# Kernel optimization log

Measured on AMD Instinct MI355X. Metric: run time of the kernel, lower is better.

## Reference

```python
import jax, jax.numpy as jnp
import numpy as np

NUM_ROUTES, NUM_TIME, DIM, K, C = 100000, 2016, 256, 100, 5
BATCH = 262144


def _xavier(key, shape):
    fan_in, fan_out = shape[0], shape[1]
    lim = np.sqrt(6.0 / (fan_in + fan_out))
    return jax.random.uniform(key, shape, jnp.float32, -lim, lim)


def setup_inputs() -> dict:
    key = jax.random.key(0)
    ks = jax.random.split(key, 9)
    route_idx = jax.random.randint(ks[0], (BATCH,), 0, NUM_ROUTES)
    time_idx = jax.random.randint(ks[1], (BATCH,), 0, NUM_TIME)
    route_table = _xavier(ks[2], (NUM_ROUTES, DIM))
    time_table = _xavier(ks[3], (NUM_TIME, DIM))
    w = _xavier(ks[4], (DIM, K))
    mode_a = _xavier(ks[5], (DIM, C))
    mode_b = _xavier(ks[6], (DIM, C))
    mode_bias = jnp.zeros((C, C), jnp.float32)
    fc_lim = 1.0 / np.sqrt(C * C + K)
    fc_w = jax.random.uniform(ks[7], (C * C + K, 1), jnp.float32, -fc_lim, fc_lim)
    fc_b = jax.random.uniform(ks[8], (1,), jnp.float32, -fc_lim, fc_lim)
    return {
        "route_idx": route_idx, "time_idx": time_idx,
        "route_table": route_table, "time_table": time_table,
        "w": w, "mode_a": mode_a, "mode_b": mode_b,
        "mode_bias": mode_bias, "fc_w": fc_w, "fc_b": fc_b,
    }


def reference(route_idx, time_idx, route_table, time_table, w, mode_a, mode_b, mode_bias, fc_w, fc_b):
    r = route_table[route_idx]            # [B, D]
    t = time_table[time_idx]              # [B, D]
    gcp = jax.nn.relu((r * t) @ w)        # [B, K]
    # einsum('ni,nj->nij') then contracting i with mode_a and j with mode_b
    # equals outer product of the two small projections (exact same math):
    ra = r @ mode_a                       # [B, C]
    tb = t @ mode_b                       # [B, C]
    inter = jax.nn.sigmoid(ra[:, :, None] * tb[:, None, :] + mode_bias)  # [B, C, C]
    feats = jnp.concatenate([gcp, inter.reshape(inter.shape[0], -1)], axis=1)  # [B, K + C*C]
    out = feats @ fc_w + fc_b             # [B, 1]
    return jnp.squeeze(out, axis=-1)      # [B]
```

## Files before the change

### kernel.cpp

```cpp
#include <hip/hip_runtime.h>
#include <stdint.h>

#define BATCH   262144
#define NROUTES 100000
#define NTIME   2016
#define DIM     256
#define KOUT    100
#define NTILES  7

typedef __attribute__((ext_vector_type(2))) float f32x2;
typedef __attribute__((ext_vector_type(4))) float f32x4;

#define WS_WFRAG_BYTES ((size_t)(NTILES * 8 * 64 * 8))
#define WS_RA_OFF   (WS_WFRAG_BYTES)
#define WS_TB_OFF   (WS_RA_OFF + (size_t)NROUTES * 32)
#define WS_RT8_OFF  (WS_TB_OFF + (size_t)NTIME * 32)
#define WS_TT8_OFF  (WS_RT8_OFF + (size_t)NROUTES * 256)
#define WS_NEED     (WS_TT8_OFF + (size_t)NTIME * 256)

template<int CTRL>
static __device__ __forceinline__ float dpp_add(float x) {
  int s = __builtin_amdgcn_update_dpp(0, __builtin_bit_cast(int, x), CTRL, 0xF, 0xF, true);
  return x + __builtin_bit_cast(float, s);
}
static __device__ __forceinline__ float wave_sum63(float x) {
  x = dpp_add<0x111>(x);
  x = dpp_add<0x112>(x);
  x = dpp_add<0x114>(x);
  x = dpp_add<0x118>(x);
  x = dpp_add<0x142>(x);
  x = dpp_add<0x143>(x);
  return x;
}
static __device__ __forceinline__ float sum16_all(float x) {
  x = dpp_add<0x0B1>(x);
  x = dpp_add<0x04E>(x);
  x = dpp_add<0x124>(x);
  x = dpp_add<0x128>(x);
  return x;
}
static __device__ __forceinline__ float sigm(float z) {
  return __builtin_amdgcn_rcpf(1.0f + __expf(-z));
}

template<int DO8>
__global__ __launch_bounds__(256) void prep_kernel(
    const float* __restrict__ route_table,
    const float* __restrict__ time_table,
    const float* __restrict__ w,
    const float* __restrict__ mode_a,
    const float* __restrict__ mode_b,
    uint8_t* __restrict__ ws)
{
  const int b   = blockIdx.x;
  const int tid = threadIdx.x;

  if (b < 14) {
    const int u = b * 256 + tid;
    const int lane = u & 63;
    const int frag = u >> 6;
    const int ks = frag / NTILES;
    const int nt = frag % NTILES;
    const int n  = nt * 16 + (lane & 15);
    const int k0 = ks * 32 + (lane >> 4) * 8;
    float v[8];
    #pragma unroll
    for (int j = 0; j < 8; ++j)
      v[j] = (n < KOUT) ? w[(size_t)(k0 + j) * KOUT + n] : 0.0f;
    uint32_t d0 = 0, d1 = 0;
    d0 = __builtin_amdgcn_cvt_pk_fp8_f32(v[0], v[1], d0, false);
    d0 = __builtin_amdgcn_cvt_pk_fp8_f32(v[2], v[3], d0, true);
    d1 = __builtin_amdgcn_cvt_pk_fp8_f32(v[4], v[5], d1, false);
    d1 = __builtin_amdgcn_cvt_pk_fp8_f32(v[6], v[7], d1, true);
    ((uint2*)ws)[u] = make_uint2(d0, d1);
    return;
  }

  const float* tab; const float* proj; float* outp; uint8_t* out8; int base;
  if (b < 14 + 63) {
    tab = time_table;  proj = mode_b; outp = (float*)(ws + WS_TB_OFF);
    out8 = ws + WS_TT8_OFF; base = (b - 14) * 32;
  } else {
    tab = route_table; proj = mode_a; outp = (float*)(ws + WS_RA_OFF);
    out8 = ws + WS_RT8_OFF; base = (b - 77) * 32;
  }

  const int wave = tid >> 6, lane = tid & 63;
  const int perm = (2 * (lane >> 4) + ((lane >> 1) & 1)) * 8 +
                   ((lane >> 2) & 3) * 2 + (lane & 1);

  float A[4][5];
  #pragma unroll
  for (int j = 0; j < 4; ++j)
    #pragma unroll
    for (int i = 0; i < 5; ++i)
      A[j][i] = proj[(4 * perm + j) * 5 + i];

  const int row0 = base + wave * 8;
  float4 v[8];
  #pragma unroll
  for (int rr = 0; rr < 8; ++rr)
    v[rr] = *(const float4*)(tab + (size_t)(row0 + rr) * DIM + 4 * perm);

  #pragma unroll
  for (int rr = 0; rr < 8; ++rr) {
    const int row = row0 + rr;
    if (DO8) {
      uint32_t u = 0;
      u = __builtin_amdgcn_cvt_pk_fp8_f32(8.f * v[rr].x, 8.f * v[rr].y, u, false);
      u = __builtin_amdgcn_cvt_pk_fp8_f32(8.f * v[rr].z, 8.f * v[rr].w, u, true);
      *(uint32_t*)(out8 + (size_t)row * 256 + 4 * lane) = u;
    }
    float p[5];
    #pragma unroll
    for (int i = 0; i < 5; ++i) {
      float s = v[rr].x * A[0][i] + v[rr].y * A[1][i] + v[rr].z * A[2][i] + v[rr].w * A[3][i];
      p[i] = wave_sum63(s);
    }
    if (lane == 63) {
      float* o = outp + (size_t)row * 8;
      *(f32x4*)o = (f32x4){p[0], p[1], p[2], p[3]};
      o[4] = p[4];
    }
  }
}

__global__ __launch_bounds__(256, 3) void main_pipelined(
    const int*   __restrict__ route_idx,
    const int*   __restrict__ time_idx,
    const float* __restrict__ mode_bias,
    const float* __restrict__ fc_w,
    const float* __restrict__ fc_b,
    const uint8_t* __restrict__ ws,
    float* __restrict__ out)
{
  __shared__ uint4 wlds[1792];
  const int tid  = threadIdx.x;
  const int wave = tid >> 6, lane = tid & 63;
  const int col  = lane & 15, quad = lane >> 4;
  const int base = (blockIdx.x * 4 + wave) * 64;

  int ri[4], ti[4];
  #pragma unroll
  for (int t = 0; t < 4; ++t) {
    ri[t] = route_idx[base + t * 16 + col];
    ti[t] = time_idx[base + t * 16 + col];
  }

  {
    const uint4* wsrc = (const uint4*)ws;
    #pragma unroll
    for (int j = 0; j < 7; ++j)
      wlds[j * 256 + tid] = wsrc[j * 256 + tid];
  }

  float fcw_l[NTILES];
  #pragma unroll
  for (int nt = 0; nt < NTILES; ++nt) {
    const int n = nt * 16 + col;
    fcw_l[nt] = (n < KOUT) ? fc_w[n] * 0.015625f : 0.0f;
  }
  const float fb = fc_b[0];

  uint4 rw[2][4], tw[2][4];
  auto issue = [&](int buf, int t) {
    const uint8_t* rb = ws + WS_RT8_OFF + (size_t)ri[t] * 256 + quad * 16;
    const uint8_t* tb = ws + WS_TT8_OFF + (size_t)ti[t] * 256 + quad * 16;
    #pragma unroll
    for (int i = 0; i < 4; ++i) {
      rw[buf][i] = *(const uint4*)(rb + i * 64);
      tw[buf][i] = *(const uint4*)(tb + i * 64);
    }
  };

  issue(0, 0);
  __syncthreads();

  const uint2* wl2 = (const uint2*)wlds;

  #pragma unroll
  for (int it = 0; it < 4; ++it) {
    const int cb = it & 1, nb = cb ^ 1;

    const float* rap = (const float*)(ws + WS_RA_OFF) + (size_t)ri[it] * 8;
    const float* tbp = (const float*)(ws + WS_TB_OFF) + (size_t)ti[it] * 8;
    f32x4 ra0 = *(const f32x4*)rap; float ra4 = rap[4];
    f32x4 tb0 = *(const f32x4*)tbp; float tb4 = tbp[4];
    if (it < 3) issue(nb, it + 1);

    f32x4 acc[NTILES];
    #pragma unroll
    for (int nt = 0; nt < NTILES; ++nt) acc[nt] = (f32x4){0.f, 0.f, 0.f, 0.f};

    #pragma unroll
    for (int ks = 0; ks < 8; ++ks) {
      const int i = ks >> 1;
      const uint32_t ra = (ks & 1) ? rw[cb][i].z : rw[cb][i].x;
      const uint32_t rb = (ks & 1) ? rw[cb][i].w : rw[cb][i].y;
      const uint32_t ta = (ks & 1) ? tw[cb][i].z : tw[cb][i].x;
      const uint32_t tb = (ks & 1) ? tw[cb][i].w : tw[cb][i].y;
      f32x2 r01 = __builtin_amdgcn_cvt_pk_f32_fp8(ra, false);
      f32x2 r23 = __builtin_amdgcn_cvt_pk_f32_fp8(ra, true);
      f32x2 r45 = __builtin_amdgcn_cvt_pk_f32_fp8(rb, false);
      f32x2 r67 = __builtin_amdgcn_cvt_pk_f32_fp8(rb, true);
      f32x2 t01 = __builtin_amdgcn_cvt_pk_f32_fp8(ta, false);
      f32x2 t23 = __builtin_amdgcn_cvt_pk_f32_fp8(ta, true);
      f32x2 t45 = __builtin_amdgcn_cvt_pk_f32_fp8(tb, false);
      f32x2 t67 = __builtin_amdgcn_cvt_pk_f32_fp8(tb, true);
      f32x2 x01 = r01 * t01, x23 = r23 * t23, x45 = r45 * t45, x67 = r67 * t67;
      uint32_t p0 = 0, p1 = 0;
      p0 = __builtin_amdgcn_cvt_pk_fp8_f32(x01.x, x01.y, p0, false);
      p0 = __builtin_amdgcn_cvt_pk_fp8_f32(x23.x, x23.y, p0, true);
      p1 = __builtin_amdgcn_cvt_pk_fp8_f32(x45.x, x45.y, p1, false);
      p1 = __builtin_amdgcn_cvt_pk_fp8_f32(x67.x, x67.y, p1, true);
      const long a64 = __builtin_bit_cast(long, make_uint2(p0, p1));
      #pragma unroll
      for (int nt = 0; nt < NTILES; ++nt) {
        const long b64 = __builtin_bit_cast(long, wl2[(ks * NTILES + nt) * 64 + lane]);
        acc[nt] = __builtin_amdgcn_mfma_f32_16x16x32_fp8_fp8(a64, b64, acc[nt], 0, 0, 0);
      }
    }

    float s[4];
    #pragma unroll
    for (int reg = 0; reg < 4; ++reg) {
      float v = 0.f;
      #pragma unroll
      for (int nt = 0; nt < NTILES; ++nt)
        v += fmaxf(acc[nt][reg], 0.f) * fcw_l[nt];
      s[reg] = sum16_all(v);
    }

    const float rav[5] = {ra0.x, ra0.y, ra0.z, ra0.w, ra4};
    const float tbv[5] = {tb0.x, tb0.y, tb0.z, tb0.w, tb4};
    const float rq = (quad & 2) ? ((quad & 1) ? rav[3] : rav[2])
                                : ((quad & 1) ? rav[1] : rav[0]);
    const float tq = (quad & 2) ? ((quad & 1) ? tbv[3] : tbv[2])
                                : ((quad & 1) ? tbv[1] : tbv[0]);
    float sig = 0.f;
    #pragma unroll
    for (int j = 0; j < 5; ++j)
      sig += sigm(rq * tbv[j] + mode_bias[5 * quad + j]) * fc_w[KOUT + 5 * quad + j];
    sig += sigm(rav[4] * tq + mode_bias[20 + quad]) * fc_w[KOUT + 20 + quad];
    if (quad == 0)
      sig += sigm(rav[4] * tbv[4] + mode_bias[24]) * fc_w[KOUT + 24];
    sig += __shfl_xor(sig, 16, 64);
    sig += __shfl_xor(sig, 32, 64);

    if (quad == (col >> 2)) {
      const float sa = (col & 1) ? s[1] : s[0];
      const float sb = (col & 1) ? s[3] : s[2];
      const float gcp = (col & 2) ? sb : sa;
      out[base + it * 16 + col] = fb + gcp + sig;
    }
  }
}

__global__ __launch_bounds__(256, 4) void main_fallback(
    const int*   __restrict__ route_idx,
    const int*   __restrict__ time_idx,
    const float* __restrict__ route_table,
    const float* __restrict__ time_table,
    const float* __restrict__ mode_bias,
    const float* __restrict__ fc_w,
    const float* __restrict__ fc_b,
    const uint8_t* __restrict__ ws,
    float* __restrict__ out)
{
  __shared__ uint4 wlds[1792];
  const int tid  = threadIdx.x;
  const int wave = tid >> 6, lane = tid & 63;
  const int col  = lane & 15, quad = lane >> 4;
  const int m0   = blockIdx.x * 64 + wave * 16;
  const size_t ri = (size_t)route_idx[m0 + col];
  const size_t ti = (size_t)time_idx[m0 + col];

  const float* rap = (const float*)(ws + WS_RA_OFF) + ri * 8;
  const float* tbp = (const float*)(ws + WS_TB_OFF) + ti * 8;
  f32x4 ra0 = *(const f32x4*)rap; float ra4 = rap[4];
  f32x4 tb0 = *(const f32x4*)tbp; float tb4 = tbp[4];

  {
    const uint4* wsrc = (const uint4*)ws;
    #pragma unroll
    for (int j = 0; j < 7; ++j)
      wlds[j * 256 + tid] = wsrc[j * 256 + tid];
  }
  __syncthreads();

  float fcw_l[NTILES];
  #pragma unroll
  for (int nt = 0; nt < NTILES; ++nt) {
    const int n = nt * 16 + col;
    fcw_l[nt] = (n < KOUT) ? fc_w[n] * 0.015625f : 0.0f;
  }

  f32x4 acc[NTILES];
  #pragma unroll
  for (int nt = 0; nt < NTILES; ++nt) acc[nt] = (f32x4){0.f, 0.f, 0.f, 0.f};
  const uint2* wl2 = (const uint2*)wlds;

  #pragma unroll
  for (int ks = 0; ks < 8; ++ks) {
    const float4* rp = (const float4*)(route_table + ri * DIM + ks * 32 + quad * 8);
    const float4* tp = (const float4*)(time_table  + ti * DIM + ks * 32 + quad * 8);
    float4 r0 = rp[0], r1 = rp[1], t0 = tp[0], t1 = tp[1];
    uint32_t p0 = 0, p1 = 0;
    p0 = __builtin_amdgcn_cvt_pk_fp8_f32(64.f * r0.x * t0.x, 64.f * r0.y * t0.y, p0, false);
    p0 = __builtin_amdgcn_cvt_pk_fp8_f32(64.f * r0.z * t0.z, 64.f * r0.w * t0.w, p0, true);
    p1 = __builtin_amdgcn_cvt_pk_fp8_f32(64.f * r1.x * t1.x, 64.f * r1.y * t1.y, p1, false);
    p1 = __builtin_amdgcn_cvt_pk_fp8_f32(64.f * r1.z * t1.z, 64.f * r1.w * t1.w, p1, true);
    const long a64 = __builtin_bit_cast(long, make_uint2(p0, p1));
    #pragma unroll
    for (int nt = 0; nt < NTILES; ++nt) {
      const long b64 = __builtin_bit_cast(long, wl2[(ks * NTILES + nt) * 64 + lane]);
      acc[nt] = __builtin_amdgcn_mfma_f32_16x16x32_fp8_fp8(a64, b64, acc[nt], 0, 0, 0);
    }
  }

  float s[4];
  #pragma unroll
  for (int reg = 0; reg < 4; ++reg) {
    float v = 0.f;
    #pragma unroll
    for (int nt = 0; nt < NTILES; ++nt)
      v += fmaxf(acc[nt][reg], 0.f) * fcw_l[nt];
    s[reg] = sum16_all(v);
  }

  const float rav[5] = {ra0.x, ra0.y, ra0.z, ra0.w, ra4};
  const float tbv[5] = {tb0.x, tb0.y, tb0.z, tb0.w, tb4};
  const float rq = (quad & 2) ? ((quad & 1) ? rav[3] : rav[2])
                              : ((quad & 1) ? rav[1] : rav[0]);
  const float tq = (quad & 2) ? ((quad & 1) ? tbv[3] : tbv[2])
                              : ((quad & 1) ? tbv[1] : tbv[0]);
  float sig = 0.f;
  #pragma unroll
  for (int j = 0; j < 5; ++j)
    sig += sigm(rq * tbv[j] + mode_bias[5 * quad + j]) * fc_w[KOUT + 5 * quad + j];
  sig += sigm(rav[4] * tq + mode_bias[20 + quad]) * fc_w[KOUT + 20 + quad];
  if (quad == 0)
    sig += sigm(rav[4] * tbv[4] + mode_bias[24]) * fc_w[KOUT + 24];
  sig += __shfl_xor(sig, 16, 64);
  sig += __shfl_xor(sig, 32, 64);

  if (quad == (col >> 2)) {
    const float sa = (col & 1) ? s[1] : s[0];
    const float sb = (col & 1) ? s[3] : s[2];
    const float gcp = (col & 2) ? sb : sa;
    out[m0 + col] = fc_b[0] + gcp + sig;
  }
}

extern "C" void kernel_launch(void* const* d_in, const int* in_sizes, int n_in,
                              void* d_out, int out_size, void* d_ws, size_t ws_size,
                              hipStream_t stream)
{
  const int*   route_idx   = (const int*)d_in[0];
  const int*   time_idx    = (const int*)d_in[1];
  const float* route_table = (const float*)d_in[2];
  const float* time_table  = (const float*)d_in[3];
  const float* w           = (const float*)d_in[4];
  const float* mode_a      = (const float*)d_in[5];
  const float* mode_b      = (const float*)d_in[6];
  const float* mode_bias   = (const float*)d_in[7];
  const float* fc_w        = (const float*)d_in[8];
  const float* fc_b        = (const float*)d_in[9];
  uint8_t* ws  = (uint8_t*)d_ws;
  float*   out = (float*)d_out;

  const int big = (ws_size >= WS_NEED) ? 1 : 0;

  if (big) {
    prep_kernel<1><<<3202, 256, 0, stream>>>(route_table, time_table, w,
                                             mode_a, mode_b, ws);
    main_pipelined<<<BATCH / 256, 256, 0, stream>>>(route_idx, time_idx,
                                                    mode_bias, fc_w, fc_b, ws, out);
  } else {
    prep_kernel<0><<<3202, 256, 0, stream>>>(route_table, time_table, w,
                                             mode_a, mode_b, ws);
    main_fallback<<<BATCH / 64, 256, 0, stream>>>(route_idx, time_idx,
                                                  route_table, time_table,
                                                  mode_bias, fc_w, fc_b, ws, out);
  }
}
```

Measured before the change: 201.9 us.

## Bucket-sort batch by route index before the main gather kernel

Adds a counting sort (histogram, scan, atomic scatter) that groups batch rows into bins of 64 route ids, storing a packed route/time key and the original row index. The main kernel then reads the sorted keys so nearby waves gather nearby fp8 route rows, improving cache locality, and scatters results back through the saved index. This costs three extra small kernels, a memset, atomics and a scattered output write.

```diff
diff --git a/kernel.cpp b/kernel.cpp
--- a/kernel.cpp
+++ b/kernel.cpp
@@ -7,6 +7,7 @@
 #define DIM     256
 #define KOUT    100
 #define NTILES  7
+#define NBINS   1568
 
 typedef __attribute__((ext_vector_type(2))) float f32x2;
 typedef __attribute__((ext_vector_type(4))) float f32x4;
@@ -16,7 +17,11 @@
 #define WS_TB_OFF   (WS_RA_OFF + (size_t)NROUTES * 32)
 #define WS_RT8_OFF  (WS_TB_OFF + (size_t)NTIME * 32)
 #define WS_TT8_OFF  (WS_RT8_OFF + (size_t)NROUTES * 256)
-#define WS_NEED     (WS_TT8_OFF + (size_t)NTIME * 256)
+#define WS_KEY_OFF  (WS_TT8_OFF + (size_t)NTIME * 256)
+#define WS_N_OFF    (WS_KEY_OFF + (size_t)BATCH * 4)
+#define WS_BIN_OFF  (WS_N_OFF + (size_t)BATCH * 4)
+#define WS_CUR_OFF  (WS_BIN_OFF + (size_t)NBINS * 4)
+#define WS_NEED     (WS_CUR_OFF + (size_t)NBINS * 4)
 
 template<int CTRL>
 static __device__ __forceinline__ float dpp_add(float x) {
@@ -41,6 +46,55 @@
 }
 static __device__ __forceinline__ float sigm(float z) {
   return __builtin_amdgcn_rcpf(1.0f + __expf(-z));
+}
+
+__global__ __launch_bounds__(256) void sort_hist(
+    const int* __restrict__ route_idx, uint32_t* __restrict__ bincnt)
+{
+  const int i = blockIdx.x * 256 + threadIdx.x;
+  if (i < BATCH) atomicAdd(&bincnt[((uint32_t)route_idx[i]) >> 6], 1u);
+}
+
+__global__ __launch_bounds__(256) void sort_scan(
+    const uint32_t* __restrict__ bincnt, uint32_t* __restrict__ cursor)
+{
+  __shared__ uint32_t part[256];
+  const int t = threadIdx.x;
+  uint32_t loc[7];
+  uint32_t s = 0;
+  #pragma unroll
+  for (int i = 0; i < 7; ++i) {
+    const int b = t * 7 + i;
+    loc[i] = (b < NBINS) ? bincnt[b] : 0u;
+    s += loc[i];
+  }
+  part[t] = s;
+  __syncthreads();
+  if (t == 0) {
+    uint32_t run = 0;
+    for (int i = 0; i < 256; ++i) { uint32_t v = part[i]; part[i] = run; run += v; }
+  }
+  __syncthreads();
+  uint32_t run = part[t];
+  #pragma unroll
+  for (int i = 0; i < 7; ++i) {
+    const int b = t * 7 + i;
+    if (b < NBINS) { cursor[b] = run; run += loc[i]; }
+  }
+}
+
+__global__ __launch_bounds__(256) void sort_scatter(
+    const int* __restrict__ route_idx, const int* __restrict__ time_idx,
+    uint32_t* __restrict__ cursor,
+    uint32_t* __restrict__ key, uint32_t* __restrict__ nn)
+{
+  const int i = blockIdx.x * 256 + threadIdx.x;
+  if (i < BATCH) {
+    const uint32_t r = (uint32_t)route_idx[i];
+    const uint32_t p = atomicAdd(&cursor[r >> 6], 1u);
+    key[p] = (r << 11) | (uint32_t)time_idx[i];
+    nn[p]  = (uint32_t)i;
+  }
 }
 
 template<int DO8>
@@ -126,8 +180,6 @@
 }
 
 __global__ __launch_bounds__(256, 3) void main_pipelined(
-    const int*   __restrict__ route_idx,
-    const int*   __restrict__ time_idx,
     const float* __restrict__ mode_bias,
     const float* __restrict__ fc_w,
     const float* __restrict__ fc_b,
@@ -140,11 +192,16 @@
   const int col  = lane & 15, quad = lane >> 4;
   const int base = (blockIdx.x * 4 + wave) * 64;
 
-  int ri[4], ti[4];
+  const uint32_t* skey = (const uint32_t*)(ws + WS_KEY_OFF);
+  const uint32_t* snn  = (const uint32_t*)(ws + WS_N_OFF);
+
+  int ri[4], ti[4]; uint32_t on[4];
   #pragma unroll
   for (int t = 0; t < 4; ++t) {
-    ri[t] = route_idx[base + t * 16 + col];
-    ti[t] = time_idx[base + t * 16 + col];
+    const uint32_t k = skey[base + t * 16 + col];
+    ri[t] = (int)(k >> 11);
+    ti[t] = (int)(k & 2047u);
+    on[t] = snn[base + t * 16 + col];
   }
 
   {
@@ -251,7 +308,7 @@
       const float sa = (col & 1) ? s[1] : s[0];
       const float sb = (col & 1) ? s[3] : s[2];
       const float gcp = (col & 2) ? sb : sa;
-      out[base + it * 16 + col] = fb + gcp + sig;
+      out[on[it]] = fb + gcp + sig;
     }
   }
 }
@@ -372,10 +429,20 @@
   const int big = (ws_size >= WS_NEED) ? 1 : 0;
 
   if (big) {
+    uint32_t* bincnt = (uint32_t*)(ws + WS_BIN_OFF);
+    uint32_t* cursor = (uint32_t*)(ws + WS_CUR_OFF);
+    uint32_t* key    = (uint32_t*)(ws + WS_KEY_OFF);
+    uint32_t* nn     = (uint32_t*)(ws + WS_N_OFF);
+
+    hipMemsetAsync(bincnt, 0, NBINS * 4, stream);
+    sort_hist<<<BATCH / 256, 256, 0, stream>>>(route_idx, bincnt);
+    sort_scan<<<1, 256, 0, stream>>>(bincnt, cursor);
+    sort_scatter<<<BATCH / 256, 256, 0, stream>>>(route_idx, time_idx,
+                                                  cursor, key, nn);
     prep_kernel<1><<<3202, 256, 0, stream>>>(route_table, time_table, w,
                                              mode_a, mode_b, ws);
-    main_pipelined<<<BATCH / 256, 256, 0, stream>>>(route_idx, time_idx,
-                                                    mode_bias, fc_w, fc_b, ws, out);
+    main_pipelined<<<BATCH / 256, 256, 0, stream>>>(mode_bias, fc_w, fc_b,
+                                                    ws, out);
   } else {
     prep_kernel<0><<<3202, 256, 0, stream>>>(route_table, time_table, w,
                                              mode_a, mode_b, ws);
```

Measured after the change: 292.5 us. +44.9%, slower.
